# Performance work log

Hardware: AMD Instinct MI355X
Metric: run time of the kernel (lower is better)

Reference implementation:

```python
import jax, jax.numpy as jnp
import numpy as np

B, S, D_MODEL, N_HEADS, D_K, D_V = 2, 2048, 1024, 16, 64, 64
LN_EPS = 1e-5


def setup_inputs() -> dict:
    key = jax.random.key(0)
    ks = jax.random.split(key, 10)
    scale = 1.0 / np.sqrt(D_MODEL)
    inp = {
        "input_Q": jax.random.normal(ks[0], (B, S, D_MODEL), jnp.float32),
        "input_K": jax.random.normal(ks[1], (B, S, D_MODEL), jnp.float32),
        "input_V": jax.random.normal(ks[2], (B, S, D_MODEL), jnp.float32),
        # causal mask (True = masked), as produced by attn_mask() with no pad tokens
        "attn_mask": jnp.broadcast_to(
            jnp.triu(jnp.ones((S, S), dtype=bool), k=1), (B, S, S)
        ),
        # weights stored [in, out] (equivalent to torch Linear weight.T)
        "W_Q": jax.random.normal(ks[3], (D_MODEL, N_HEADS * D_K), jnp.float32) * scale,
        "W_K": jax.random.normal(ks[4], (D_MODEL, N_HEADS * D_K), jnp.float32) * scale,
        "W_V": jax.random.normal(ks[5], (D_MODEL, N_HEADS * D_V), jnp.float32) * scale,
        "W_O": jax.random.normal(ks[6], (N_HEADS * D_V, D_MODEL), jnp.float32) * scale,
        "ln_gamma": jnp.ones((D_MODEL,), jnp.float32),
        "ln_beta": jnp.zeros((D_MODEL,), jnp.float32),
    }
    return inp


def _layernorm(x, gamma, beta):
    mu = jnp.mean(x, axis=-1, keepdims=True)
    var = jnp.var(x, axis=-1, keepdims=True)
    return (x - mu) * jax.lax.rsqrt(var + LN_EPS) * gamma + beta


def reference(input_Q, input_K, input_V, attn_mask, W_Q, W_K, W_V, W_O, ln_gamma, ln_beta):
    b = input_Q.shape[0]
    # projections -> [B, H, S, d]
    Q = (input_Q @ W_Q).reshape(b, -1, N_HEADS, D_K).transpose(0, 2, 1, 3)
    K = (input_K @ W_K).reshape(b, -1, N_HEADS, D_K).transpose(0, 2, 1, 3)
    V = (input_V @ W_V).reshape(b, -1, N_HEADS, D_V).transpose(0, 2, 1, 3)
    scores = jnp.einsum("bhqd,bhkd->bhqk", Q, K) / np.sqrt(D_K)
    scores = jnp.where(attn_mask[:, None, :, :], jnp.float32(-1e9), scores)
    attn = jax.nn.softmax(scores, axis=-1)
    context = jnp.einsum("bhqk,bhkd->bhqd", attn, V)
    context = context.transpose(0, 2, 1, 3).reshape(b, -1, N_HEADS * D_V)
    output = context @ W_O
    out = _layernorm(output + input_Q, ln_gamma, ln_beta)
    return out, attn
```

## Files before the change

kernel.cpp:

```cpp
#include <hip/hip_runtime.h>
#include <stdint.h>

typedef unsigned short u16;
typedef __attribute__((ext_vector_type(8))) short short8;
typedef __attribute__((ext_vector_type(4))) float f32x4;
typedef __attribute__((ext_vector_type(4))) unsigned short u16x4;
typedef __attribute__((ext_vector_type(4))) unsigned int uint4v;

#define MFMA16(a,b,c) __builtin_amdgcn_mfma_f32_16x16x32_bf16((a),(b),(c),0,0,0)

__device__ __forceinline__ void gload16(const void* g, void* l) {
  __builtin_amdgcn_global_load_lds(
      (__attribute__((address_space(1))) void*)(uintptr_t)(g),
      (__attribute__((address_space(3))) void*)(uint32_t)(uintptr_t)(l),
      16, 0, 0);
}

__device__ __forceinline__ u16 f2bf(float x) {
  union { float f; unsigned u; } v; v.f = x;
  unsigned r = v.u + 0x7fffu + ((v.u >> 16) & 1u);
  return (u16)(r >> 16);
}
__device__ __forceinline__ unsigned pack2(float a, float b) {
  return (unsigned)f2bf(a) | ((unsigned)f2bf(b) << 16);
}

__global__ __launch_bounds__(256) void cast_x(const float* x0, const float* x1, const float* x2,
                                              u16* y0, u16* y1, u16* y2) {
  const float* x; u16* y;
  if (blockIdx.y == 0)      { x = x0; y = y0; }
  else if (blockIdx.y == 1) { x = x1; y = y1; }
  else                      { x = x2; y = y2; }
  size_t i = ((size_t)blockIdx.x * 256 + threadIdx.x) * 4;
  float4 v = *(const float4*)(x + i);
  u16x4 o; o[0] = f2bf(v.x); o[1] = f2bf(v.y); o[2] = f2bf(v.z); o[3] = f2bf(v.w);
  *(u16x4*)(y + i) = o;
}

__global__ __launch_bounds__(256) void trans_w(const float* w0, const float* w1, const float* w2, const float* w3,
                                               u16* t0, u16* t1, u16* t2, u16* t3) {
  const float* W; u16* T;
  switch (blockIdx.z) {
    case 0:  W = w0; T = t0; break;
    case 1:  W = w1; T = t1; break;
    case 2:  W = w2; T = t2; break;
    default: W = w3; T = t3; break;
  }
  __shared__ float tile[32][33];
  int k0 = blockIdx.x * 32, n0 = blockIdx.y * 32;
  int tx = threadIdx.x, ty = threadIdx.y;
#pragma unroll
  for (int j = 0; j < 4; ++j)
    tile[ty + 8*j][tx] = W[(size_t)(k0 + ty + 8*j) * 1024 + n0 + tx];
  __syncthreads();
#pragma unroll
  for (int j = 0; j < 4; ++j)
    T[(size_t)(n0 + ty + 8*j) * 1024 + k0 + tx] = f2bf(tile[tx][ty + 8*j]);
}

__device__ __forceinline__ void gemm_stage(const u16* A, const u16* BT, int row0, int col0,
                                           int tid, int w, int kt, char* la, char* lb) {
#pragma unroll
  for (int j = 0; j < 2; ++j) {
    int c = j * 256 + tid;
    int mr = c & 127, kc = c >> 7;
    gload16(A  + (size_t)(row0 + mr) * 1024 + kt*32 + kc*8, la + (j*4 + w) * 1024);
    gload16(BT + (size_t)(col0 + mr) * 1024 + kt*32 + kc*8, lb + (j*4 + w) * 1024);
  }
}

__device__ __forceinline__ void gemm_core(const u16* A, const u16* BT, int row0, int col0,
                                          char* ldsA, char* ldsB, f32x4 (&acc)[4][4]) {
  int tid = threadIdx.x, w = tid >> 6, lane = tid & 63;
  int u = lane >> 4, c16 = lane & 15, wr = w >> 1, wc = w & 1;
  gemm_stage(A, BT, row0, col0, tid, w, 0, ldsA, ldsB);
  asm volatile("s_waitcnt vmcnt(0)" ::: "memory");
  __syncthreads();
  for (int kt = 0; kt < 32; ++kt) {
    int cur = kt & 1;
    if (kt < 31)
      gemm_stage(A, BT, row0, col0, tid, w, kt + 1, ldsA + (cur^1)*8192, ldsB + (cur^1)*8192);
    const char* la = ldsA + cur * 8192;
    const char* lb = ldsB + cur * 8192;
    short8 af[4], bv[4];
#pragma unroll
    for (int i = 0; i < 4; ++i) {
      af[i] = *(const short8*)(la + (u*128 + wr*64 + i*16 + c16) * 16);
      bv[i] = *(const short8*)(lb + (u*128 + wc*64 + i*16 + c16) * 16);
    }
#pragma unroll
    for (int i = 0; i < 4; ++i)
#pragma unroll
      for (int n = 0; n < 4; ++n)
        acc[i][n] = MFMA16(af[i], bv[n], acc[i][n]);
    asm volatile("s_waitcnt vmcnt(0)" ::: "memory");
    __syncthreads();
  }
}

__global__ __launch_bounds__(256) void gemm_qkv(const u16* Xq, const u16* Xk, const u16* Xv,
                                                const u16* WTq, const u16* WTk, const u16* WTv,
                                                u16* Qh, u16* Kh, u16* VhT) {
  __shared__ char ldsA[16384], ldsB[16384];
  int z = blockIdx.z;
  const u16* A  = (z == 0) ? Xq  : ((z == 1) ? Xk  : Xv);
  const u16* BT = (z == 0) ? WTq : ((z == 1) ? WTk : WTv);
  int row0 = blockIdx.x * 128, col0 = blockIdx.y * 128;
  f32x4 acc[4][4] = {};
  gemm_core(A, BT, row0, col0, ldsA, ldsB, acc);
  int tid = threadIdx.x, w = tid >> 6, lane = tid & 63, u = lane >> 4, c16 = lane & 15;
  int wr = w >> 1, wc = w & 1;
#pragma unroll
  for (int i = 0; i < 4; ++i)
#pragma unroll
    for (int n = 0; n < 4; ++n)
#pragma unroll
      for (int r = 0; r < 4; ++r) {
        int row = row0 + wr*64 + i*16 + u*4 + r;
        int colg = col0 + wc*64 + n*16 + c16;
        int b = row >> 11, s = row & 2047;
        int h = colg >> 6, d = colg & 63;
        float v = acc[i][n][r];
        if (z == 0)      Qh[((size_t)(b*16 + h) * 2048 + s) * 64 + d] = f2bf(v * 0.125f);
        else if (z == 1) Kh[((size_t)(b*16 + h) * 2048 + s) * 64 + d] = f2bf(v);
        else             VhT[((size_t)(b*16 + h) * 64 + d) * 2048 + s] = f2bf(v);
      }
}

__global__ __launch_bounds__(256) void gemm_out(const u16* Ctx, const u16* WTo,
                                                const float* resid, float* outF) {
  __shared__ char ldsA[16384], ldsB[16384];
  int row0 = blockIdx.x * 128, col0 = blockIdx.y * 128;
  f32x4 acc[4][4] = {};
  gemm_core(Ctx, WTo, row0, col0, ldsA, ldsB, acc);
  int tid = threadIdx.x, w = tid >> 6, lane = tid & 63, u = lane >> 4, c16 = lane & 15;
  int wr = w >> 1, wc = w & 1;
#pragma unroll
  for (int i = 0; i < 4; ++i)
#pragma unroll
    for (int n = 0; n < 4; ++n)
#pragma unroll
      for (int r = 0; r < 4; ++r) {
        int row = row0 + wr*64 + i*16 + u*4 + r;
        int colg = col0 + wc*64 + n*16 + c16;
        size_t idx = (size_t)row * 1024 + colg;
        outF[idx] = acc[i][n][r] + resid[idx];
      }
}

__device__ __forceinline__ void qk_tile(const char* Kbuf, short8 qf0, short8 qf1,
                                        int cq, int u, int rho, f32x4 (&acc)[4]) {
#pragma unroll
  for (int st = 0; st < 4; ++st) {
    short8 a0 = *(const short8*)(Kbuf + (st*16 + cq) * 128 + ((u*16) ^ rho));
    short8 a1 = *(const short8*)(Kbuf + (st*16 + cq) * 128 + ((64 + u*16) ^ rho));
    acc[st] = MFMA16(a0, qf0, acc[st]);
    acc[st] = MFMA16(a1, qf1, acc[st]);
  }
}

__device__ __forceinline__ void stage_k64(const u16* pan, int kt, char* buf, int tid, int w) {
#pragma unroll
  for (int j = 0; j < 2; ++j) {
    int c = j * 256 + tid;
    int row = c >> 3;
    int cc = (c & 7) ^ (row & 7);
    gload16(pan + (size_t)(kt*64 + row) * 64 + cc*8, buf + (j*4 + w) * 1024);
  }
}
__device__ __forceinline__ void stage_v64(const u16* vpan, int kt, char* buf, int tid, int w) {
#pragma unroll
  for (int j = 0; j < 2; ++j) {
    int c = j * 256 + tid;
    int d = c >> 3;
    int cc = (c & 7) ^ (d & 7);
    gload16(vpan + (size_t)d * 2048 + kt*64 + cc*8, buf + (j*4 + w) * 1024);
  }
}

__device__ __forceinline__ void tile_pass1(const char* Kcur, short8 qf0, short8 qf1,
                                           int q, int q0t, int kt, int ktd_t,
                                           int cq, int u, int rho, float& ls) {
  f32x4 acc[4] = {};
  qk_tile(Kcur, qf0, qf1, cq, u, rho, acc);
  if (kt == ktd_t) {
#pragma unroll
    for (int st = 0; st < 4; ++st)
#pragma unroll
      for (int r = 0; r < 4; ++r) {
        int key = q0t + st*16 + u*4 + r;
        if (key > q) acc[st][r] = -1e30f;
      }
  }
#pragma unroll
  for (int st = 0; st < 4; ++st)
#pragma unroll
    for (int r = 0; r < 4; ++r) ls += __expf(acc[st][r]);
}

__device__ __forceinline__ void tile_pass2(const char* Kcur, const char* Vcur, float* Pw,
                                           short8 qf0, short8 qf1, int q, int q0t, int kt, int ktd_t,
                                           float rl, float* apan, int w, int u, int cq,
                                           int rho, int sw, f32x4 (&ctx)[4]) {
  f32x4 acc[4] = {};
  qk_tile(Kcur, qf0, qf1, cq, u, rho, acc);
  if (kt == ktd_t) {
#pragma unroll
    for (int st = 0; st < 4; ++st)
#pragma unroll
      for (int r = 0; r < 4; ++r) {
        int key = q0t + st*16 + u*4 + r;
        if (key > q) acc[st][r] = -1e30f;
      }
  }
#pragma unroll
  for (int st = 0; st < 4; ++st) {
    f32x4 p;
#pragma unroll
    for (int r = 0; r < 4; ++r) p[r] = __expf(acc[st][r]) * rl;
    *(f32x4*)&Pw[(cq*64 + st*16 + u*4) ^ sw] = p;
  }
  __builtin_amdgcn_sched_barrier(0);
#pragma unroll
  for (int j = 0; j < 4; ++j) {
    int row = j*4 + u;
    f32x4 v = *(const f32x4*)&Pw[(row*64 + cq*4) ^ ((row & 7) << 2)];
    __builtin_nontemporal_store(v,
        (f32x4*)(apan + (size_t)(q0t + w*16 + row) * 2048 + kt*64 + cq*4));
  }
#pragma unroll
  for (int wd = 0; wd < 2; ++wd) {
    int b0 = (cq*64 + wd*32 + u*8) ^ sw;
    f32x4 pa0 = *(const f32x4*)&Pw[b0];
    f32x4 pa1 = *(const f32x4*)&Pw[b0 ^ 4];
    uint4v pk;
    pk[0] = pack2(pa0[0], pa0[1]);
    pk[1] = pack2(pa0[2], pa0[3]);
    pk[2] = pack2(pa1[0], pa1[1]);
    pk[3] = pack2(pa1[2], pa1[3]);
    union { uint4v u4; short8 s8; } cvt; cvt.u4 = pk;
    short8 pa = cvt.s8;
#pragma unroll
    for (int nt = 0; nt < 4; ++nt) {
      short8 vb = *(const short8*)(Vcur + (nt*16 + cq) * 128 + ((wd*64 + u*16) ^ rho));
      ctx[nt] = MFMA16(pa, vb, ctx[nt]);
    }
  }
  __builtin_amdgcn_sched_barrier(0);
}

__global__ __launch_bounds__(256) void attn_fused(const u16* Qh, const u16* Kh, const u16* VhT,
                                                  float* attnO, u16* Ctx) {
  __shared__ char Kl[2][8192];
  __shared__ char Vl[2][8192];
  __shared__ float Pf[4][1024];
  int tid = threadIdx.x, w = tid >> 6, lane = tid & 63;
  int u = lane >> 4, cq = lane & 15;
  int pi = blockIdx.x;
  int bh = blockIdx.y;
  int tlo = pi, thi = 31 - pi;
  int q0lo = tlo * 64, q0hi = thi * 64;
  int qlo = q0lo + w*16 + cq;
  int qhi = q0hi + w*16 + cq;
  int rho = (cq & 7) << 4;
  int sw  = (cq & 7) << 2;
  const u16* Kpan = Kh  + (size_t)bh * (2048 * 64);
  const u16* Vpan = VhT + (size_t)bh * (64 * 2048);
  const u16* Qlo = Qh + ((size_t)bh * 2048 + qlo) * 64;
  const u16* Qhi = Qh + ((size_t)bh * 2048 + qhi) * 64;
  short8 qlo0 = *(const short8*)(Qlo + u*8);
  short8 qlo1 = *(const short8*)(Qlo + 32 + u*8);
  short8 qhi0 = *(const short8*)(Qhi + u*8);
  short8 qhi1 = *(const short8*)(Qhi + 32 + u*8);

  float ls_lo = 0.f, ls_hi = 0.f;
  stage_k64(Kpan, 0, Kl[0], tid, w);
  asm volatile("s_waitcnt vmcnt(0)" ::: "memory");
  __builtin_amdgcn_s_barrier();
  asm volatile("" ::: "memory");
  for (int kt = 0; kt <= thi; ++kt) {
    int cur = kt & 1;
    if (kt < thi) stage_k64(Kpan, kt + 1, Kl[cur ^ 1], tid, w);
    __builtin_amdgcn_sched_barrier(0);
    tile_pass1(Kl[cur], qhi0, qhi1, qhi, q0hi, kt, thi, cq, u, rho, ls_hi);
    if (kt <= tlo)
      tile_pass1(Kl[cur], qlo0, qlo1, qlo, q0lo, kt, tlo, cq, u, rho, ls_lo);
    if (kt < thi) {
      asm volatile("s_waitcnt vmcnt(0)" ::: "memory");
      __builtin_amdgcn_s_barrier();
      asm volatile("" ::: "memory");
    }
  }
  ls_lo += __shfl_xor(ls_lo, 16);  ls_lo += __shfl_xor(ls_lo, 32);
  ls_hi += __shfl_xor(ls_hi, 16);  ls_hi += __shfl_xor(ls_hi, 32);
  float rl_lo = 1.f / ls_lo, rl_hi = 1.f / ls_hi;

  asm volatile("" ::: "memory");
  __builtin_amdgcn_s_barrier();
  asm volatile("" ::: "memory");

  f32x4 ctx_lo[4] = {}, ctx_hi[4] = {};
  float* apan = attnO + (size_t)bh * 2048 * 2048;
  float* Pw = Pf[w];
  stage_k64(Kpan, 0, Kl[0], tid, w);
  stage_v64(Vpan, 0, Vl[0], tid, w);
  asm volatile("s_waitcnt vmcnt(0)" ::: "memory");
  __builtin_amdgcn_s_barrier();
  asm volatile("" ::: "memory");
  for (int kt = 0; kt <= thi; ++kt) {
    int cur = kt & 1;
    if (kt < thi) {
      stage_k64(Kpan, kt + 1, Kl[cur ^ 1], tid, w);
      stage_v64(Vpan, kt + 1, Vl[cur ^ 1], tid, w);
    }
    __builtin_amdgcn_sched_barrier(0);
    tile_pass2(Kl[cur], Vl[cur], Pw, qhi0, qhi1, qhi, q0hi, kt, thi,
               rl_hi, apan, w, u, cq, rho, sw, ctx_hi);
    bool lo_act = (kt <= tlo);
    if (lo_act)
      tile_pass2(Kl[cur], Vl[cur], Pw, qlo0, qlo1, qlo, q0lo, kt, tlo,
                 rl_lo, apan, w, u, cq, rho, sw, ctx_lo);
    if (kt < thi) {
      if (lo_act) asm volatile("s_waitcnt vmcnt(8)" ::: "memory");
      else        asm volatile("s_waitcnt vmcnt(4)" ::: "memory");
      __builtin_amdgcn_s_barrier();
      asm volatile("" ::: "memory");
    }
  }

  f32x4 z4 = {};
  for (int kt = tlo + 1; kt < 32; ++kt)
#pragma unroll
    for (int j = 0; j < 4; ++j)
      __builtin_nontemporal_store(z4,
          (f32x4*)(apan + (size_t)(q0lo + w*16 + j*4 + u) * 2048 + kt*64 + cq*4));
  for (int kt = thi + 1; kt < 32; ++kt)
#pragma unroll
    for (int j = 0; j < 4; ++j)
      __builtin_nontemporal_store(z4,
          (f32x4*)(apan + (size_t)(q0hi + w*16 + j*4 + u) * 2048 + kt*64 + cq*4));

  int b = bh >> 4, h = bh & 15;
#pragma unroll
  for (int nt = 0; nt < 4; ++nt)
#pragma unroll
    for (int r = 0; r < 4; ++r) {
      int qr = q0lo + w*16 + u*4 + r;
      Ctx[((size_t)b * 2048 + qr) * 1024 + h*64 + nt*16 + cq] = f2bf(ctx_lo[nt][r]);
    }
#pragma unroll
  for (int nt = 0; nt < 4; ++nt)
#pragma unroll
    for (int r = 0; r < 4; ++r) {
      int qr = q0hi + w*16 + u*4 + r;
      Ctx[((size_t)b * 2048 + qr) * 1024 + h*64 + nt*16 + cq] = f2bf(ctx_hi[nt][r]);
    }
}

__global__ __launch_bounds__(256) void ln_kernel(const float* X, const float* g, const float* b, float* out) {
  int row = blockIdx.x, tid = threadIdx.x;
  float4 v = *(const float4*)(X + (size_t)row * 1024 + tid * 4);
  float s  = v.x + v.y + v.z + v.w;
  float q2 = v.x*v.x + v.y*v.y + v.z*v.z + v.w*v.w;
#pragma unroll
  for (int off = 32; off; off >>= 1) { s += __shfl_xor(s, off); q2 += __shfl_xor(q2, off); }
  __shared__ float red[8];
  int w = tid >> 6, lane = tid & 63;
  if (lane == 0) { red[w] = s; red[4 + w] = q2; }
  __syncthreads();
  s  = red[0] + red[1] + red[2] + red[3];
  q2 = red[4] + red[5] + red[6] + red[7];
  float mean = s * (1.f / 1024.f);
  float var  = q2 * (1.f / 1024.f) - mean * mean;
  float rs   = rsqrtf(var + 1e-5f);
  float4 gv = *(const float4*)(g + tid * 4);
  float4 bv = *(const float4*)(b + tid * 4);
  float4 o;
  o.x = (v.x - mean) * rs * gv.x + bv.x;
  o.y = (v.y - mean) * rs * gv.y + bv.y;
  o.z = (v.z - mean) * rs * gv.z + bv.z;
  o.w = (v.w - mean) * rs * gv.w + bv.w;
  *(float4*)(out + (size_t)row * 1024 + tid * 4) = o;
}

extern "C" void kernel_launch(void* const* d_in, const int* in_sizes, int n_in,
                              void* d_out, int out_size, void* d_ws, size_t ws_size,
                              hipStream_t stream) {
  (void)in_sizes; (void)n_in; (void)out_size; (void)ws_size;
  const float* inQ = (const float*)d_in[0];
  const float* inK = (const float*)d_in[1];
  const float* inV = (const float*)d_in[2];
  const float* Wq  = (const float*)d_in[4];
  const float* Wk  = (const float*)d_in[5];
  const float* Wv  = (const float*)d_in[6];
  const float* Wo  = (const float*)d_in[7];
  const float* gam = (const float*)d_in[8];
  const float* bet = (const float*)d_in[9];
  float* out   = (float*)d_out;
  float* attnO = out + (size_t)4194304;

  char* ws = (char*)d_ws;
  u16*   WTo    = (u16*)ws;
  u16*   Qh     = (u16*)(ws + 2097152);
  u16*   Kh     = (u16*)(ws + 2097152 + (size_t)8388608);
  u16*   VhT    = (u16*)(ws + 2097152 + (size_t)2*8388608);
  u16*   Ctx    = (u16*)(ws + 2097152 + (size_t)3*8388608);
  float* OutLin = (float*)(ws + 2097152 + (size_t)4*8388608);

  u16* Xbq = (u16*)attnO;
  u16* Xbk = Xbq + (size_t)4194304;
  u16* Xbv = Xbk + (size_t)4194304;
  u16* WTq = Xbv + (size_t)4194304;
  u16* WTk = WTq + (size_t)1048576;
  u16* WTv = WTk + (size_t)1048576;

  cast_x<<<dim3(4096, 3), 256, 0, stream>>>(inQ, inK, inV, Xbq, Xbk, Xbv);
  trans_w<<<dim3(32, 32, 4), dim3(32, 8), 0, stream>>>(Wq, Wk, Wv, Wo, WTq, WTk, WTv, WTo);
  gemm_qkv<<<dim3(32, 8, 3), 256, 0, stream>>>(Xbq, Xbk, Xbv, WTq, WTk, WTv, Qh, Kh, VhT);
  attn_fused<<<dim3(16, 32), 256, 0, stream>>>(Qh, Kh, VhT, attnO, Ctx);
  gemm_out<<<dim3(32, 8), 256, 0, stream>>>(Ctx, WTo, inQ, OutLin);
  ln_kernel<<<4096, 256, 0, stream>>>(OutLin, gam, bet, out);
}
```

Measured before the change: 275.6 us.

## Triple-buffer GEMM and attention K loads, merge prep kernels, add wave priorities

Merges the input cast and weight transpose into one launch, removing a kernel launch. The GEMM main loop moves from double to triple buffering with a partial vmcnt wait, giving one barrier per iteration and a deeper prefetch. The attention first pass also triple-buffers its K tiles the same way. s_setprio is raised around the MFMA-heavy tile work. The cost is more LDS per block, which may lower occupancy, and the triple-buffer waits depend on exact vmcnt counts.

```diff
diff --git a/kernel.cpp b/kernel.cpp
--- a/kernel.cpp
+++ b/kernel.cpp
@@ -25,37 +25,38 @@
   return (unsigned)f2bf(a) | ((unsigned)f2bf(b) << 16);
 }
 
-__global__ __launch_bounds__(256) void cast_x(const float* x0, const float* x1, const float* x2,
-                                              u16* y0, u16* y1, u16* y2) {
-  const float* x; u16* y;
-  if (blockIdx.y == 0)      { x = x0; y = y0; }
-  else if (blockIdx.y == 1) { x = x1; y = y1; }
-  else                      { x = x2; y = y2; }
-  size_t i = ((size_t)blockIdx.x * 256 + threadIdx.x) * 4;
-  float4 v = *(const float4*)(x + i);
-  u16x4 o; o[0] = f2bf(v.x); o[1] = f2bf(v.y); o[2] = f2bf(v.z); o[3] = f2bf(v.w);
-  *(u16x4*)(y + i) = o;
-}
-
-__global__ __launch_bounds__(256) void trans_w(const float* w0, const float* w1, const float* w2, const float* w3,
-                                               u16* t0, u16* t1, u16* t2, u16* t3) {
-  const float* W; u16* T;
-  switch (blockIdx.z) {
-    case 0:  W = w0; T = t0; break;
-    case 1:  W = w1; T = t1; break;
-    case 2:  W = w2; T = t2; break;
-    default: W = w3; T = t3; break;
-  }
+__global__ __launch_bounds__(256) void prep_kernel(const float* x0, const float* x1, const float* x2,
+                                                   u16* y0, u16* y1, u16* y2,
+                                                   const float* w0, const float* w1, const float* w2, const float* w3,
+                                                   u16* t0, u16* t1, u16* t2, u16* t3) {
   __shared__ float tile[32][33];
-  int k0 = blockIdx.x * 32, n0 = blockIdx.y * 32;
-  int tx = threadIdx.x, ty = threadIdx.y;
-#pragma unroll
-  for (int j = 0; j < 4; ++j)
-    tile[ty + 8*j][tx] = W[(size_t)(k0 + ty + 8*j) * 1024 + n0 + tx];
-  __syncthreads();
-#pragma unroll
-  for (int j = 0; j < 4; ++j)
-    T[(size_t)(n0 + ty + 8*j) * 1024 + k0 + tx] = f2bf(tile[tx][ty + 8*j]);
+  int z = blockIdx.y;
+  if (z < 3) {
+    const float* x = (z == 0) ? x0 : ((z == 1) ? x1 : x2);
+    u16*         y = (z == 0) ? y0 : ((z == 1) ? y1 : y2);
+    size_t i = ((size_t)blockIdx.x * 256 + threadIdx.x) * 4;
+    float4 v = *(const float4*)(x + i);
+    u16x4 o; o[0] = f2bf(v.x); o[1] = f2bf(v.y); o[2] = f2bf(v.z); o[3] = f2bf(v.w);
+    *(u16x4*)(y + i) = o;
+  } else {
+    if (blockIdx.x >= 1024) return;
+    const float* W; u16* T;
+    switch (z - 3) {
+      case 0:  W = w0; T = t0; break;
+      case 1:  W = w1; T = t1; break;
+      case 2:  W = w2; T = t2; break;
+      default: W = w3; T = t3; break;
+    }
+    int k0 = (blockIdx.x >> 5) * 32, n0 = (blockIdx.x & 31) * 32;
+    int tx = threadIdx.x & 31, ty = threadIdx.x >> 5;
+#pragma unroll
+    for (int j = 0; j < 4; ++j)
+      tile[ty + 8*j][tx] = W[(size_t)(k0 + ty + 8*j) * 1024 + n0 + tx];
+    __syncthreads();
+#pragma unroll
+    for (int j = 0; j < 4; ++j)
+      T[(size_t)(n0 + ty + 8*j) * 1024 + k0 + tx] = f2bf(tile[tx][ty + 8*j]);
+  }
 }
 
 __device__ __forceinline__ void gemm_stage(const u16* A, const u16* BT, int row0, int col0,
@@ -74,12 +75,18 @@
   int tid = threadIdx.x, w = tid >> 6, lane = tid & 63;
   int u = lane >> 4, c16 = lane & 15, wr = w >> 1, wc = w & 1;
   gemm_stage(A, BT, row0, col0, tid, w, 0, ldsA, ldsB);
-  asm volatile("s_waitcnt vmcnt(0)" ::: "memory");
-  __syncthreads();
+  gemm_stage(A, BT, row0, col0, tid, w, 1, ldsA + 8192, ldsB + 8192);
+  int cur = 0;
   for (int kt = 0; kt < 32; ++kt) {
-    int cur = kt & 1;
-    if (kt < 31)
-      gemm_stage(A, BT, row0, col0, tid, w, kt + 1, ldsA + (cur^1)*8192, ldsB + (cur^1)*8192);
+    if (kt < 31) asm volatile("s_waitcnt vmcnt(4)" ::: "memory");
+    else         asm volatile("s_waitcnt vmcnt(0)" ::: "memory");
+    __builtin_amdgcn_s_barrier();
+    asm volatile("" ::: "memory");
+    if (kt < 30) {
+      int nb = cur + 2; if (nb >= 3) nb -= 3;
+      gemm_stage(A, BT, row0, col0, tid, w, kt + 2, ldsA + nb*8192, ldsB + nb*8192);
+    }
+    __builtin_amdgcn_sched_barrier(0);
     const char* la = ldsA + cur * 8192;
     const char* lb = ldsB + cur * 8192;
     short8 af[4], bv[4];
@@ -93,15 +100,14 @@
 #pragma unroll
       for (int n = 0; n < 4; ++n)
         acc[i][n] = MFMA16(af[i], bv[n], acc[i][n]);
-    asm volatile("s_waitcnt vmcnt(0)" ::: "memory");
-    __syncthreads();
+    cur = cur + 1; if (cur >= 3) cur = 0;
   }
 }
 
 __global__ __launch_bounds__(256) void gemm_qkv(const u16* Xq, const u16* Xk, const u16* Xv,
                                                 const u16* WTq, const u16* WTk, const u16* WTv,
                                                 u16* Qh, u16* Kh, u16* VhT) {
-  __shared__ char ldsA[16384], ldsB[16384];
+  __shared__ char ldsA[24576], ldsB[24576];
   int z = blockIdx.z;
   const u16* A  = (z == 0) ? Xq  : ((z == 1) ? Xk  : Xv);
   const u16* BT = (z == 0) ? WTq : ((z == 1) ? WTk : WTv);
@@ -129,7 +135,7 @@
 
 __global__ __launch_bounds__(256) void gemm_out(const u16* Ctx, const u16* WTo,
                                                 const float* resid, float* outF) {
-  __shared__ char ldsA[16384], ldsB[16384];
+  __shared__ char ldsA[24576], ldsB[24576];
   int row0 = blockIdx.x * 128, col0 = blockIdx.y * 128;
   f32x4 acc[4][4] = {};
   gemm_core(Ctx, WTo, row0, col0, ldsA, ldsB, acc);
@@ -203,6 +209,7 @@
                                            float rl, float* apan, int w, int u, int cq,
                                            int rho, int sw, f32x4 (&ctx)[4]) {
   f32x4 acc[4] = {};
+  __builtin_amdgcn_s_setprio(1);
   qk_tile(Kcur, qf0, qf1, cq, u, rho, acc);
   if (kt == ktd_t) {
 #pragma unroll
@@ -246,12 +253,13 @@
       ctx[nt] = MFMA16(pa, vb, ctx[nt]);
     }
   }
+  __builtin_amdgcn_s_setprio(0);
   __builtin_amdgcn_sched_barrier(0);
 }
 
 __global__ __launch_bounds__(256) void attn_fused(const u16* Qh, const u16* Kh, const u16* VhT,
                                                   float* attnO, u16* Ctx) {
-  __shared__ char Kl[2][8192];
+  __shared__ char Kl[3][8192];
   __shared__ char Vl[2][8192];
   __shared__ float Pf[4][1024];
   int tid = threadIdx.x, w = tid >> 6, lane = tid & 63;
@@ -275,21 +283,24 @@
 
   float ls_lo = 0.f, ls_hi = 0.f;
   stage_k64(Kpan, 0, Kl[0], tid, w);
-  asm volatile("s_waitcnt vmcnt(0)" ::: "memory");
-  __builtin_amdgcn_s_barrier();
-  asm volatile("" ::: "memory");
+  stage_k64(Kpan, 1, Kl[1], tid, w);
+  int cur1 = 0;
   for (int kt = 0; kt <= thi; ++kt) {
-    int cur = kt & 1;
-    if (kt < thi) stage_k64(Kpan, kt + 1, Kl[cur ^ 1], tid, w);
+    if (kt < thi) asm volatile("s_waitcnt vmcnt(4)" ::: "memory");
+    else          asm volatile("s_waitcnt vmcnt(0)" ::: "memory");
+    __builtin_amdgcn_s_barrier();
+    asm volatile("" ::: "memory");
+    if (kt + 2 <= thi) {
+      int nb = cur1 + 2; if (nb >= 3) nb -= 3;
+      stage_k64(Kpan, kt + 2, Kl[nb], tid, w);
+    }
     __builtin_amdgcn_sched_barrier(0);
-    tile_pass1(Kl[cur], qhi0, qhi1, qhi, q0hi, kt, thi, cq, u, rho, ls_hi);
+    __builtin_amdgcn_s_setprio(1);
+    tile_pass1(Kl[cur1], qhi0, qhi1, qhi, q0hi, kt, thi, cq, u, rho, ls_hi);
     if (kt <= tlo)
-      tile_pass1(Kl[cur], qlo0, qlo1, qlo, q0lo, kt, tlo, cq, u, rho, ls_lo);
-    if (kt < thi) {
-      asm volatile("s_waitcnt vmcnt(0)" ::: "memory");
-      __builtin_amdgcn_s_barrier();
-      asm volatile("" ::: "memory");
-    }
+      tile_pass1(Kl[cur1], qlo0, qlo1, qlo, q0lo, kt, tlo, cq, u, rho, ls_lo);
+    __builtin_amdgcn_s_setprio(0);
+    cur1 = cur1 + 1; if (cur1 >= 3) cur1 = 0;
   }
   ls_lo += __shfl_xor(ls_lo, 16);  ls_lo += __shfl_xor(ls_lo, 32);
   ls_hi += __shfl_xor(ls_hi, 16);  ls_hi += __shfl_xor(ls_hi, 32);
@@ -414,8 +425,8 @@
   u16* WTk = WTq + (size_t)1048576;
   u16* WTv = WTk + (size_t)1048576;
 
-  cast_x<<<dim3(4096, 3), 256, 0, stream>>>(inQ, inK, inV, Xbq, Xbk, Xbv);
-  trans_w<<<dim3(32, 32, 4), dim3(32, 8), 0, stream>>>(Wq, Wk, Wv, Wo, WTq, WTk, WTv, WTo);
+  prep_kernel<<<dim3(4096, 7), 256, 0, stream>>>(inQ, inK, inV, Xbq, Xbk, Xbv,
+                                                 Wq, Wk, Wv, Wo, WTq, WTk, WTv, WTo);
   gemm_qkv<<<dim3(32, 8, 3), 256, 0, stream>>>(Xbq, Xbk, Xbv, WTq, WTk, WTv, Qh, Kh, VhT);
   attn_fused<<<dim3(16, 32), 256, 0, stream>>>(Qh, Kh, VhT, attnO, Ctx);
   gemm_out<<<dim3(32, 8), 256, 0, stream>>>(Ctx, WTo, inQ, OutLin);
```

After: 269.2 us. 1.02x faster.
